# Kernel optimization log

Hardware: AMD Instinct MI355X
Metric: run time of the kernel (lower is better)

Reference implementation:

```python
import jax, jax.numpy as jnp
import numpy as np

D_MODEL = 1024
NUM_HEADS = 16
D_HEAD = D_MODEL // NUM_HEADS
LN_EPS = 1e-5
ROPE_BASE = 10000.0


def layer_norm(x, w, b=None, eps=LN_EPS):
    mu = jnp.mean(x, axis=-1, keepdims=True)
    var = jnp.mean(jnp.square(x - mu), axis=-1, keepdims=True)
    y = (x - mu) * jax.lax.rsqrt(var + eps) * w
    return y + b if b is not None else y


def _rotate_half(x):
    x1, x2 = jnp.split(x, 2, axis=-1)
    return jnp.concatenate([-x2, x1], axis=-1)


def apply_rotary(q, k):
    # q, k: [B, S, H, Dh]
    s, dh = q.shape[1], q.shape[-1]
    inv_freq = 1.0 / (ROPE_BASE ** (jnp.arange(0, dh, 2, dtype=jnp.float32) / dh))
    t = jnp.arange(s, dtype=jnp.float32)
    freqs = jnp.outer(t, inv_freq)                      # [S, Dh/2]
    emb = jnp.concatenate([freqs, freqs], axis=-1)      # [S, Dh]
    cos = jnp.cos(emb)[None, :, None, :].astype(q.dtype)
    sin = jnp.sin(emb)[None, :, None, :].astype(q.dtype)
    q_rot = q * cos + _rotate_half(q) * sin
    k_rot = k * cos + _rotate_half(k) * sin
    return q_rot, k_rot


def setup_inputs() -> dict:
    key = jax.random.key(0)
    ks = jax.random.split(key, 8)
    B, L, D = 4, 2048, D_MODEL
    x = jax.random.normal(ks[0], (B, L, D), dtype=jnp.float32)
    sequence_id = jnp.sort(jax.random.randint(ks[1], (B, L), 0, 8), axis=-1).astype(jnp.int64)
    scale = 1.0 / np.sqrt(D)
    return {
        "x": x,
        "sequence_id": sequence_id,
        "ln_w": jnp.ones((D,), jnp.float32),
        "ln_b": jnp.zeros((D,), jnp.float32),
        "w_qkv": jax.random.normal(ks[2], (D, 3 * D), jnp.float32) * scale,
        "q_ln_w": jnp.ones((D,), jnp.float32),
        "k_ln_w": jnp.ones((D,), jnp.float32),
        "w_out": jax.random.normal(ks[3], (D, D), jnp.float32) * scale,
    }


def reference(x, sequence_id, ln_w, ln_b, w_qkv, q_ln_w, k_ln_w, w_out):
    B, L, D = x.shape
    H, Dh = NUM_HEADS, D_HEAD
    # fused LayerNorm + QKV projection
    qkv = layer_norm(x, ln_w, ln_b) @ w_qkv              # [B, L, 3D]
    q, k, v = jnp.split(qkv, 3, axis=-1)
    # qk layernorm (scale only, bias=False)
    q = layer_norm(q, q_ln_w)
    k = layer_norm(k, k_ln_w)
    # split heads and apply rotary
    q = q.reshape(B, L, H, Dh)
    k = k.reshape(B, L, H, Dh)
    q, k = apply_rotary(q, k)
    v = v.reshape(B, L, H, Dh)
    # packed-sequence mask: tokens attend only within same sequence id
    mask = (sequence_id[:, :, None] == sequence_id[:, None, :])[:, None, :, :]  # [B,1,L,L]
    scale = 1.0 / np.sqrt(Dh)
    scores = jnp.einsum("bqhd,bkhd->bhqk", q, k) * scale
    scores = jnp.where(mask, scores, jnp.finfo(scores.dtype).min)
    attn = jax.nn.softmax(scores, axis=-1)
    ctx = jnp.einsum("bhqk,bkhd->bqhd", attn, v).reshape(B, L, D)
    return ctx @ w_out
```

## Files before the change

### kernel.cpp

```cpp
#include <hip/hip_runtime.h>
#include <hip/hip_bf16.h>
#include <cstdint>
#include <cstddef>
#include <type_traits>

#define D_MODEL 1024
#define NH      16
#define DH      64
#define LSEQ    2048
#define BATCH   4
#define NTOK    8192
#define K3      3072

typedef __attribute__((ext_vector_type(8))) short  short8;
typedef __attribute__((ext_vector_type(4))) float  floatx4;

__device__ __forceinline__ unsigned short f2bf_bits(float f) {
  __hip_bfloat16 h = __float2bfloat16(f);
  return __builtin_bit_cast(unsigned short, h);
}
__device__ __forceinline__ float bf2f(unsigned short u) {
  return __bfloat162float(__builtin_bit_cast(__hip_bfloat16, u));
}
__device__ __forceinline__ unsigned int pack_bf16(float lo, float hi) {
  return (unsigned int)f2bf_bits(lo) | ((unsigned int)f2bf_bits(hi) << 16);
}

__device__ __forceinline__ void gld_lds16(const void* g, void* l) {
  __builtin_amdgcn_global_load_lds(
      (const __attribute__((address_space(1))) void*)g,
      (__attribute__((address_space(3))) void*)l,
      16, 0, 0);
}

__global__ __launch_bounds__(256)
void transpose_cast(const float* __restrict__ src, __hip_bfloat16* __restrict__ dst,
                    int R, int C) {
  __shared__ float tile[32][33];
  const int c0 = blockIdx.x * 32, r0 = blockIdx.y * 32;
  const int x = threadIdx.x, y = threadIdx.y;
  #pragma unroll
  for (int j = 0; j < 32; j += 8)
    tile[y + j][x] = src[(size_t)(r0 + y + j) * C + c0 + x];
  __syncthreads();
  #pragma unroll
  for (int j = 0; j < 32; j += 8)
    dst[(size_t)(c0 + y + j) * R + r0 + x] = __float2bfloat16(tile[x][y + j]);
}

__global__ __launch_bounds__(256)
void ln_kernel(const float* __restrict__ x, const float* __restrict__ w,
               const float* __restrict__ bb, __hip_bfloat16* __restrict__ h) {
  const int t = blockIdx.x, tid = threadIdx.x;
  const float4 v = reinterpret_cast<const float4*>(x + (size_t)t * D_MODEL)[tid];
  float s  = v.x + v.y + v.z + v.w;
  float ss = v.x*v.x + v.y*v.y + v.z*v.z + v.w*v.w;
  #pragma unroll
  for (int off = 32; off > 0; off >>= 1) {
    s  += __shfl_down(s, off);
    ss += __shfl_down(ss, off);
  }
  __shared__ float red[8];
  if ((tid & 63) == 0) { red[(tid >> 6) * 2] = s; red[(tid >> 6) * 2 + 1] = ss; }
  __syncthreads();
  s  = red[0] + red[2] + red[4] + red[6];
  ss = red[1] + red[3] + red[5] + red[7];
  const float mu  = s * (1.f / D_MODEL);
  const float var = ss * (1.f / D_MODEL) - mu * mu;
  const float rs  = rsqrtf(var + 1e-5f);
  const float4 wv = reinterpret_cast<const float4*>(w)[tid];
  const float4 bv = reinterpret_cast<const float4*>(bb)[tid];
  ushort4 o;
  o.x = f2bf_bits((v.x - mu) * rs * wv.x + bv.x);
  o.y = f2bf_bits((v.y - mu) * rs * wv.y + bv.y);
  o.z = f2bf_bits((v.z - mu) * rs * wv.z + bv.z);
  o.w = f2bf_bits((v.w - mu) * rs * wv.w + bv.w);
  reinterpret_cast<ushort4*>(h + (size_t)t * D_MODEL)[tid] = o;
}

template <typename OutT>
__global__ __launch_bounds__(256, 2)
void gemm_bt(const __hip_bfloat16* __restrict__ A, const __hip_bfloat16* __restrict__ Bt,
             OutT* __restrict__ C, int M, int N, int K) {
  const int tid  = threadIdx.x;
  const int lane = tid & 63;
  const int wave = tid >> 6;
  const int bm = blockIdx.y * 128;
  const int bn = blockIdx.x * 128;
  const int wm = (wave & 1) * 64;
  const int wn = (wave >> 1) * 64;
  const int quad = lane >> 4;
  const int l16  = lane & 15;

  __shared__ __align__(16) __hip_bfloat16 As[128 * 64];
  __shared__ __align__(16) __hip_bfloat16 Bs[128 * 64];

  floatx4 acc[4][4];
  #pragma unroll
  for (int i = 0; i < 4; i++)
    #pragma unroll
    for (int j = 0; j < 4; j++) {
      floatx4 z = {0.f, 0.f, 0.f, 0.f};
      acc[i][j] = z;
    }

  const int srow = tid >> 3;
  const int sq   = tid & 7;
  const int sc8  = (sq ^ (srow & 7)) * 8;
  const __hip_bfloat16* Ab = A  + (size_t)(bm + srow) * K + sc8;
  const __hip_bfloat16* Bb = Bt + (size_t)(bn + srow) * K + sc8;

  const int axr = l16 & 7;

  for (int k0 = 0; k0 < K; k0 += 64) {
    __syncthreads();
    #pragma unroll
    for (int p = 0; p < 4; p++) {
      gld_lds16(Ab + (size_t)(p * 32) * K + k0, (char*)As + p * 4096 + tid * 16);
      gld_lds16(Bb + (size_t)(p * 32) * K + k0, (char*)Bs + p * 4096 + tid * 16);
    }
    __syncthreads();
    #pragma unroll
    for (int s0 = 0; s0 < 2; s0++) {
      const int qo = ((s0 * 4 + quad) ^ axr) * 8;
      short8 af[4], bfr[4];
      #pragma unroll
      for (int i = 0; i < 4; i++)
        af[i] = *reinterpret_cast<const short8*>(As + (wm + i * 16 + l16) * 64 + qo);
      #pragma unroll
      for (int j = 0; j < 4; j++)
        bfr[j] = *reinterpret_cast<const short8*>(Bs + (wn + j * 16 + l16) * 64 + qo);
      #pragma unroll
      for (int i = 0; i < 4; i++)
        #pragma unroll
        for (int j = 0; j < 4; j++)
          acc[i][j] = __builtin_amdgcn_mfma_f32_16x16x32_bf16(af[i], bfr[j], acc[i][j], 0, 0, 0);
    }
  }

  #pragma unroll
  for (int i = 0; i < 4; i++)
    #pragma unroll
    for (int j = 0; j < 4; j++) {
      const int row0 = bm + wm + i * 16 + quad * 4;
      const int col  = bn + wn + j * 16 + l16;
      #pragma unroll
      for (int r = 0; r < 4; r++) {
        if constexpr (std::is_same<OutT, __hip_bfloat16>::value)
          C[(size_t)(row0 + r) * N + col] = __float2bfloat16(acc[i][j][r]);
        else
          C[(size_t)(row0 + r) * N + col] = acc[i][j][r];
      }
    }
}

__global__ __launch_bounds__(256)
void seg_kernel(const int* __restrict__ sid, int* __restrict__ segstart,
                int* __restrict__ segend) {
  const int i = blockIdx.x * 256 + threadIdx.x;
  const int b = i >> 11, l = i & 2047;
  const int* row = sid + (size_t)b * LSEQ;
  const int v = row[l];
  int lo = 0, hi = l;
  while (lo < hi) { int mid = (lo + hi) >> 1; if (row[mid] < v) lo = mid + 1; else hi = mid; }
  segstart[i] = lo;
  lo = l + 1; hi = LSEQ;
  while (lo < hi) { int mid = (lo + hi) >> 1; if (row[mid] <= v) lo = mid + 1; else hi = mid; }
  segend[i] = lo;
}

__global__ __launch_bounds__(256)
void rope_kernel(const unsigned short* __restrict__ qkv, const float* __restrict__ qw,
                 const float* __restrict__ kw, unsigned short* __restrict__ qT,
                 unsigned short* __restrict__ kT) {
  const int t = blockIdx.x, tid = threadIdx.x;
  const int b = t >> 11, l = t & 2047;
  const unsigned short* row = qkv + (size_t)t * K3;
  const ushort4 qu = reinterpret_cast<const ushort4*>(row)[tid];
  const ushort4 ku = reinterpret_cast<const ushort4*>(row + 1024)[tid];
  const float4 q4 = make_float4(bf2f(qu.x), bf2f(qu.y), bf2f(qu.z), bf2f(qu.w));
  const float4 k4 = make_float4(bf2f(ku.x), bf2f(ku.y), bf2f(ku.z), bf2f(ku.w));
  float qs  = q4.x + q4.y + q4.z + q4.w;
  float qss = q4.x*q4.x + q4.y*q4.y + q4.z*q4.z + q4.w*q4.w;
  float ks  = k4.x + k4.y + k4.z + k4.w;
  float kss = k4.x*k4.x + k4.y*k4.y + k4.z*k4.z + k4.w*k4.w;
  #pragma unroll
  for (int off = 32; off > 0; off >>= 1) {
    qs  += __shfl_down(qs, off);  qss += __shfl_down(qss, off);
    ks  += __shfl_down(ks, off);  kss += __shfl_down(kss, off);
  }
  __shared__ float red[16];
  const int w = tid >> 6;
  if ((tid & 63) == 0) {
    red[w*4] = qs; red[w*4+1] = qss; red[w*4+2] = ks; red[w*4+3] = kss;
  }
  __syncthreads();
  qs  = red[0] + red[4] + red[8]  + red[12];
  qss = red[1] + red[5] + red[9]  + red[13];
  ks  = red[2] + red[6] + red[10] + red[14];
  kss = red[3] + red[7] + red[11] + red[15];
  const float qmu = qs * (1.f/1024), qvar = qss * (1.f/1024) - qmu*qmu;
  const float qrs = rsqrtf(qvar + 1e-5f);
  const float kmu = ks * (1.f/1024), kvar = kss * (1.f/1024) - kmu*kmu;
  const float krs = rsqrtf(kvar + 1e-5f);

  __shared__ float qn[1024];
  __shared__ float kn[1024];
  const float4 qwv = reinterpret_cast<const float4*>(qw)[tid];
  const float4 kwv = reinterpret_cast<const float4*>(kw)[tid];
  const int d = tid * 4;
  qn[d+0] = (q4.x - qmu) * qrs * qwv.x;
  qn[d+1] = (q4.y - qmu) * qrs * qwv.y;
  qn[d+2] = (q4.z - qmu) * qrs * qwv.z;
  qn[d+3] = (q4.w - qmu) * qrs * qwv.w;
  kn[d+0] = (k4.x - kmu) * krs * kwv.x;
  kn[d+1] = (k4.y - kmu) * krs * kwv.y;
  kn[d+2] = (k4.z - kmu) * krs * kwv.z;
  kn[d+3] = (k4.w - kmu) * krs * kwv.w;
  __syncthreads();

  const int hh = d >> 6, dh = d & 63;
  float oq[4], ok[4];
  #pragma unroll
  for (int i = 0; i < 4; i++) {
    const int dd = dh + i;
    const int j = dd & 31;
    const float th = (float)l * __expf(-(float)j * 0.28782313662425575f);
    const float cs = cosf(th), sn = sinf(th);
    const float qp = (dd < 32) ? -qn[d + i + 32] : qn[d + i - 32];
    const float kp = (dd < 32) ? -kn[d + i + 32] : kn[d + i - 32];
    oq[i] = (qn[d + i] * cs + qp * sn) * 0.125f;
    ok[i] = kn[d + i] * cs + kp * sn;
  }
  const size_t ob = ((size_t)(b * NH + hh) * LSEQ + l) * DH + dh;
  ushort4 pq, pk;
  pq.x = f2bf_bits(oq[0]); pq.y = f2bf_bits(oq[1]); pq.z = f2bf_bits(oq[2]); pq.w = f2bf_bits(oq[3]);
  pk.x = f2bf_bits(ok[0]); pk.y = f2bf_bits(ok[1]); pk.z = f2bf_bits(ok[2]); pk.w = f2bf_bits(ok[3]);
  *reinterpret_cast<ushort4*>(qT + ob) = pq;
  *reinterpret_cast<ushort4*>(kT + ob) = pk;
}

__global__ __launch_bounds__(256)
void vtrans(const unsigned short* __restrict__ qkv, unsigned short* __restrict__ vT) {
  __shared__ __align__(16) unsigned short T[64 * 72];
  const int bh = blockIdx.y;
  const int b = bh >> 4, h = bh & 15;
  const int l0 = blockIdx.x * 64;
  const int tid = threadIdx.x;
  #pragma unroll
  for (int it = 0; it < 2; it++) {
    const int cid = tid + it * 256;
    const int r = cid >> 3, c = (cid & 7) * 8;
    *reinterpret_cast<short8*>(T + r * 72 + c) =
        *reinterpret_cast<const short8*>(qkv + (size_t)(b * LSEQ + l0 + r) * K3
                                         + 2048 + h * DH + c);
  }
  __syncthreads();
  #pragma unroll
  for (int it = 0; it < 2; it++) {
    const int cid = tid + it * 256;
    const int dh = cid >> 3, c = (cid & 7) * 8;
    short8 o;
    #pragma unroll
    for (int e = 0; e < 8; e++) o[e] = (short)T[(c + e) * 72 + dh];
    *reinterpret_cast<short8*>(vT + ((size_t)bh * DH + dh) * LSEQ + l0 + c) = o;
  }
}

__global__ __launch_bounds__(256)
void attn_mfma(const unsigned short* __restrict__ qT, const unsigned short* __restrict__ kT,
               const unsigned short* __restrict__ vT, const int* __restrict__ segs,
               const int* __restrict__ sege, unsigned short* __restrict__ ctx) {
  const int tid  = threadIdx.x;
  const int lane = tid & 63, w = tid >> 6;
  const int quad = lane >> 4, l16 = lane & 15;
  const int qbase = blockIdx.x * 64;
  const int h = blockIdx.y, b = blockIdx.z;
  const int qy = qbase + w * 16 + l16;
  const size_t bh = (size_t)(b * NH + h);
  const unsigned short* Kg = kT + bh * LSEQ * DH;
  const unsigned short* Vg = vT + bh * DH * LSEQ;

  __shared__ __align__(16) unsigned short Ks[64 * 72];
  __shared__ __align__(16) unsigned short Vs[64 * 72];
  __shared__ __align__(16) unsigned short Ps[4][16 * 72];

  const unsigned short* Qrow = qT + (bh * LSEQ + qy) * DH;
  const short8 qf0 = *reinterpret_cast<const short8*>(Qrow + quad * 8);
  const short8 qf1 = *reinterpret_cast<const short8*>(Qrow + 32 + quad * 8);

  const int st = segs[b * LSEQ + qy];
  const int en = sege[b * LSEQ + qy];
  const unsigned span = (unsigned)(en - st);
  const int kmin = segs[b * LSEQ + qbase] & ~63;
  const int kmax = sege[b * LSEQ + qbase + 63];
  const int wmin = segs[b * LSEQ + qbase + w * 16];
  const int wmax = sege[b * LSEQ + qbase + w * 16 + 15];

  floatx4 acc[4];
  #pragma unroll
  for (int dt = 0; dt < 4; dt++) { floatx4 z = {0.f,0.f,0.f,0.f}; acc[dt] = z; }
  float m = -1e30f, lsum = 0.f;

  const int r_ = tid >> 3, c_ = (tid & 7) * 8;

  for (int kk = kmin; kk < kmax; kk += 64) {
    __syncthreads();
    #pragma unroll
    for (int it = 0; it < 2; it++) {
      const int r = r_ + it * 32;
      *reinterpret_cast<short8*>(Ks + r * 72 + c_) =
          *reinterpret_cast<const short8*>(Kg + (size_t)(kk + r) * DH + c_);
      *reinterpret_cast<short8*>(Vs + r * 72 + c_) =
          *reinterpret_cast<const short8*>(Vg + (size_t)r * LSEQ + kk + c_);
    }
    __syncthreads();

    if (kk + 64 <= wmin || kk >= wmax) continue;

    floatx4 sc[4];
    #pragma unroll
    for (int t = 0; t < 4; t++) {
      const short8 kf0 = *reinterpret_cast<const short8*>(Ks + (t * 16 + l16) * 72 + quad * 8);
      const short8 kf1 = *reinterpret_cast<const short8*>(Ks + (t * 16 + l16) * 72 + 32 + quad * 8);
      floatx4 z = {0.f,0.f,0.f,0.f};
      sc[t] = __builtin_amdgcn_mfma_f32_16x16x32_bf16(kf0, qf0, z, 0, 0, 0);
      sc[t] = __builtin_amdgcn_mfma_f32_16x16x32_bf16(kf1, qf1, sc[t], 0, 0, 0);
    }

    float vm = -1e30f;
    #pragma unroll
    for (int t = 0; t < 4; t++) {
      const int k0 = kk + t * 16 + quad * 4;
      #pragma unroll
      for (int r = 0; r < 4; r++) {
        const bool ok = (unsigned)(k0 + r - st) < span;
        sc[t][r] = ok ? sc[t][r] : -1e30f;
        vm = fmaxf(vm, sc[t][r]);
      }
    }
    vm = fmaxf(vm, __shfl_xor(vm, 16));
    vm = fmaxf(vm, __shfl_xor(vm, 32));
    const float mn = fmaxf(m, vm);
    const float alpha = __expf(m - mn);
    m = mn;

    float rs = 0.f;
    #pragma unroll
    for (int t = 0; t < 4; t++) {
      float p0 = (sc[t][0] > -1e29f) ? __expf(sc[t][0] - mn) : 0.f;
      float p1 = (sc[t][1] > -1e29f) ? __expf(sc[t][1] - mn) : 0.f;
      float p2 = (sc[t][2] > -1e29f) ? __expf(sc[t][2] - mn) : 0.f;
      float p3 = (sc[t][3] > -1e29f) ? __expf(sc[t][3] - mn) : 0.f;
      rs += (p0 + p1) + (p2 + p3);
      uint2 pk;
      pk.x = pack_bf16(p0, p1);
      pk.y = pack_bf16(p2, p3);
      *reinterpret_cast<uint2*>(&Ps[w][l16 * 72 + t * 16 + quad * 4]) = pk;
    }
    rs += __shfl_xor(rs, 16);
    rs += __shfl_xor(rs, 32);
    lsum = lsum * alpha + rs;

    const short8 pf0 = *reinterpret_cast<const short8*>(&Ps[w][l16 * 72 + quad * 8]);
    const short8 pf1 = *reinterpret_cast<const short8*>(&Ps[w][l16 * 72 + 32 + quad * 8]);

    #pragma unroll
    for (int dt = 0; dt < 4; dt++) {
      #pragma unroll
      for (int r = 0; r < 4; r++) acc[dt][r] *= alpha;
      const short8 vf0 = *reinterpret_cast<const short8*>(Vs + (dt * 16 + l16) * 72 + quad * 8);
      const short8 vf1 = *reinterpret_cast<const short8*>(Vs + (dt * 16 + l16) * 72 + 32 + quad * 8);
      acc[dt] = __builtin_amdgcn_mfma_f32_16x16x32_bf16(vf0, pf0, acc[dt], 0, 0, 0);
      acc[dt] = __builtin_amdgcn_mfma_f32_16x16x32_bf16(vf1, pf1, acc[dt], 0, 0, 0);
    }
  }

  const float inv = (lsum > 0.f) ? 1.f / lsum : 0.f;
  unsigned short* orow = ctx + ((size_t)(b * LSEQ + qy)) * D_MODEL + h * DH;
  #pragma unroll
  for (int dt = 0; dt < 4; dt++) {
    uint2 o;
    o.x = pack_bf16(acc[dt][0] * inv, acc[dt][1] * inv);
    o.y = pack_bf16(acc[dt][2] * inv, acc[dt][3] * inv);
    *reinterpret_cast<uint2*>(orow + dt * 16 + quad * 4) = o;
  }
}

extern "C" void kernel_launch(void* const* d_in, const int* in_sizes, int n_in,
                              void* d_out, int out_size, void* d_ws, size_t ws_size,
                              hipStream_t stream) {
  const float* x      = (const float*)d_in[0];
  const int*   sid    = (const int*)d_in[1];
  const float* ln_w   = (const float*)d_in[2];
  const float* ln_b   = (const float*)d_in[3];
  const float* w_qkv  = (const float*)d_in[4];
  const float* q_ln_w = (const float*)d_in[5];
  const float* k_ln_w = (const float*)d_in[6];
  const float* w_out  = (const float*)d_in[7];
  float* out = (float*)d_out;
  char* ws = (char*)d_ws;

  constexpr size_t OFF_WQKVT = 0;
  constexpr size_t OFF_WOUTT = 6291456;
  constexpr size_t OFF_H     = 8388608;
  constexpr size_t OFF_QKV   = 25165824;
  constexpr size_t OFF_QT    = 75497472;
  constexpr size_t OFF_KT    = 92274688;
  constexpr size_t OFF_VT    = 109051904;
  constexpr size_t OFF_CTX   = 125829120;
  constexpr size_t OFF_SEGS  = 142606336;
  constexpr size_t OFF_SEGE  = 142639104;

  __hip_bfloat16* wqkvT = (__hip_bfloat16*)(ws + OFF_WQKVT);
  __hip_bfloat16* woutT = (__hip_bfloat16*)(ws + OFF_WOUTT);
  __hip_bfloat16* hbuf  = (__hip_bfloat16*)(ws + OFF_H);
  __hip_bfloat16* qkvb  = (__hip_bfloat16*)(ws + OFF_QKV);
  unsigned short* qTb   = (unsigned short*)(ws + OFF_QT);
  unsigned short* kTb   = (unsigned short*)(ws + OFF_KT);
  unsigned short* vTb   = (unsigned short*)(ws + OFF_VT);
  unsigned short* ctx   = (unsigned short*)(ws + OFF_CTX);
  int*            segst = (int*)(ws + OFF_SEGS);
  int*            segen = (int*)(ws + OFF_SEGE);

  transpose_cast<<<dim3(96, 32), dim3(32, 8), 0, stream>>>(w_qkv, wqkvT, 1024, 3072);
  transpose_cast<<<dim3(32, 32), dim3(32, 8), 0, stream>>>(w_out, woutT, 1024, 1024);
  ln_kernel<<<NTOK, 256, 0, stream>>>(x, ln_w, ln_b, hbuf);
  gemm_bt<__hip_bfloat16><<<dim3(K3 / 128, NTOK / 128), 256, 0, stream>>>(
      hbuf, wqkvT, qkvb, NTOK, K3, 1024);
  seg_kernel<<<NTOK / 256, 256, 0, stream>>>(sid, segst, segen);
  rope_kernel<<<NTOK, 256, 0, stream>>>((const unsigned short*)qkvb, q_ln_w, k_ln_w,
                                        qTb, kTb);
  vtrans<<<dim3(LSEQ / 64, BATCH * NH), 256, 0, stream>>>((const unsigned short*)qkvb, vTb);
  attn_mfma<<<dim3(LSEQ / 64, NH, BATCH), 256, 0, stream>>>(qTb, kTb, vTb, segst, segen, ctx);
  gemm_bt<float><<<dim3(D_MODEL / 128, NTOK / 128), 256, 0, stream>>>(
      (const __hip_bfloat16*)ctx, woutT, out, NTOK, D_MODEL, 1024);
}
```

Measured before the change: 279.3 us.

## Use one wave per row in LN/rope, direct-to-LDS swizzled loads, LDS seg search

LayerNorm and the qk-norm/rotary kernels now process one token per wavefront, so the reduction uses wave shuffles only, with no shared memory or block barriers. Rotary uses sincos computed per lane and broadcast by shuffle, replacing per-element cos/sin. The attention K/V tiles and the V transpose now use direct global-to-LDS loads into an XOR-swizzled 64-wide layout instead of padded register-staged copies, which saves LDS and VGPR traffic. The segment kernel caches the sequence-id row in LDS for its binary searches. The swizzle index maths must match on every read, and gld_lds16 is assumed to already exist in the part of the file not shown.

```diff
diff --git a/kernel.cpp b/kernel.cpp
--- a/kernel.cpp
+++ b/kernel.cpp
@@ -51,31 +51,38 @@
 __global__ __launch_bounds__(256)
 void ln_kernel(const float* __restrict__ x, const float* __restrict__ w,
                const float* __restrict__ bb, __hip_bfloat16* __restrict__ h) {
-  const int t = blockIdx.x, tid = threadIdx.x;
-  const float4 v = reinterpret_cast<const float4*>(x + (size_t)t * D_MODEL)[tid];
-  float s  = v.x + v.y + v.z + v.w;
-  float ss = v.x*v.x + v.y*v.y + v.z*v.z + v.w*v.w;
-  #pragma unroll
-  for (int off = 32; off > 0; off >>= 1) {
-    s  += __shfl_down(s, off);
-    ss += __shfl_down(ss, off);
-  }
-  __shared__ float red[8];
-  if ((tid & 63) == 0) { red[(tid >> 6) * 2] = s; red[(tid >> 6) * 2 + 1] = ss; }
-  __syncthreads();
-  s  = red[0] + red[2] + red[4] + red[6];
-  ss = red[1] + red[3] + red[5] + red[7];
-  const float mu  = s * (1.f / D_MODEL);
-  const float var = ss * (1.f / D_MODEL) - mu * mu;
-  const float rs  = rsqrtf(var + 1e-5f);
-  const float4 wv = reinterpret_cast<const float4*>(w)[tid];
-  const float4 bv = reinterpret_cast<const float4*>(bb)[tid];
-  ushort4 o;
-  o.x = f2bf_bits((v.x - mu) * rs * wv.x + bv.x);
-  o.y = f2bf_bits((v.y - mu) * rs * wv.y + bv.y);
-  o.z = f2bf_bits((v.z - mu) * rs * wv.z + bv.z);
-  o.w = f2bf_bits((v.w - mu) * rs * wv.w + bv.w);
-  reinterpret_cast<ushort4*>(h + (size_t)t * D_MODEL)[tid] = o;
+  const int lane = threadIdx.x & 63;
+  const int t = blockIdx.x * 4 + (threadIdx.x >> 6);
+  const float4* xr = reinterpret_cast<const float4*>(x) + (size_t)t * 256;
+  float4 v[4];
+  float s = 0.f, ss = 0.f;
+  #pragma unroll
+  for (int i = 0; i < 4; i++) {
+    v[i] = xr[lane + i * 64];
+    s  += (v[i].x + v[i].y) + (v[i].z + v[i].w);
+    ss += (v[i].x*v[i].x + v[i].y*v[i].y) + (v[i].z*v[i].z + v[i].w*v[i].w);
+  }
+  #pragma unroll
+  for (int off = 1; off < 64; off <<= 1) {
+    s  += __shfl_xor(s, off);
+    ss += __shfl_xor(ss, off);
+  }
+  const float mu = s * (1.f / 1024);
+  const float rs = rsqrtf(ss * (1.f / 1024) - mu * mu + 1e-5f);
+  const float4* wr = reinterpret_cast<const float4*>(w);
+  const float4* br = reinterpret_cast<const float4*>(bb);
+  ushort4* hr = reinterpret_cast<ushort4*>(h) + (size_t)t * 256;
+  #pragma unroll
+  for (int i = 0; i < 4; i++) {
+    const float4 wv = wr[lane + i * 64];
+    const float4 bv = br[lane + i * 64];
+    ushort4 o;
+    o.x = f2bf_bits((v[i].x - mu) * rs * wv.x + bv.x);
+    o.y = f2bf_bits((v[i].y - mu) * rs * wv.y + bv.y);
+    o.z = f2bf_bits((v[i].z - mu) * rs * wv.z + bv.z);
+    o.w = f2bf_bits((v[i].w - mu) * rs * wv.w + bv.w);
+    hr[lane + i * 64] = o;
+  }
 }
 
 template <typename OutT>
@@ -157,15 +164,22 @@
 __global__ __launch_bounds__(256)
 void seg_kernel(const int* __restrict__ sid, int* __restrict__ segstart,
                 int* __restrict__ segend) {
-  const int i = blockIdx.x * 256 + threadIdx.x;
-  const int b = i >> 11, l = i & 2047;
+  __shared__ int srow[LSEQ];
+  const int blk = blockIdx.x;
+  const int b = blk >> 3;
+  const int tid = threadIdx.x;
   const int* row = sid + (size_t)b * LSEQ;
-  const int v = row[l];
+  #pragma unroll
+  for (int i = 0; i < 8; i++) srow[tid + i * 256] = row[tid + i * 256];
+  __syncthreads();
+  const int l = (blk & 7) * 256 + tid;
+  const int v = srow[l];
   int lo = 0, hi = l;
-  while (lo < hi) { int mid = (lo + hi) >> 1; if (row[mid] < v) lo = mid + 1; else hi = mid; }
+  while (lo < hi) { int mid = (lo + hi) >> 1; if (srow[mid] < v) lo = mid + 1; else hi = mid; }
+  const int i = b * LSEQ + l;
   segstart[i] = lo;
   lo = l + 1; hi = LSEQ;
-  while (lo < hi) { int mid = (lo + hi) >> 1; if (row[mid] <= v) lo = mid + 1; else hi = mid; }
+  while (lo < hi) { int mid = (lo + hi) >> 1; if (srow[mid] <= v) lo = mid + 1; else hi = mid; }
   segend[i] = lo;
 }
 
@@ -173,96 +187,101 @@
 void rope_kernel(const unsigned short* __restrict__ qkv, const float* __restrict__ qw,
                  const float* __restrict__ kw, unsigned short* __restrict__ qT,
                  unsigned short* __restrict__ kT) {
-  const int t = blockIdx.x, tid = threadIdx.x;
+  const int lane = threadIdx.x & 63;
+  const int t = blockIdx.x * 4 + (threadIdx.x >> 6);
   const int b = t >> 11, l = t & 2047;
   const unsigned short* row = qkv + (size_t)t * K3;
-  const ushort4 qu = reinterpret_cast<const ushort4*>(row)[tid];
-  const ushort4 ku = reinterpret_cast<const ushort4*>(row + 1024)[tid];
-  const float4 q4 = make_float4(bf2f(qu.x), bf2f(qu.y), bf2f(qu.z), bf2f(qu.w));
-  const float4 k4 = make_float4(bf2f(ku.x), bf2f(ku.y), bf2f(ku.z), bf2f(ku.w));
-  float qs  = q4.x + q4.y + q4.z + q4.w;
-  float qss = q4.x*q4.x + q4.y*q4.y + q4.z*q4.z + q4.w*q4.w;
-  float ks  = k4.x + k4.y + k4.z + k4.w;
-  float kss = k4.x*k4.x + k4.y*k4.y + k4.z*k4.z + k4.w*k4.w;
-  #pragma unroll
-  for (int off = 32; off > 0; off >>= 1) {
-    qs  += __shfl_down(qs, off);  qss += __shfl_down(qss, off);
-    ks  += __shfl_down(ks, off);  kss += __shfl_down(kss, off);
-  }
-  __shared__ float red[16];
-  const int w = tid >> 6;
-  if ((tid & 63) == 0) {
-    red[w*4] = qs; red[w*4+1] = qss; red[w*4+2] = ks; red[w*4+3] = kss;
-  }
-  __syncthreads();
-  qs  = red[0] + red[4] + red[8]  + red[12];
-  qss = red[1] + red[5] + red[9]  + red[13];
-  ks  = red[2] + red[6] + red[10] + red[14];
-  kss = red[3] + red[7] + red[11] + red[15];
-  const float qmu = qs * (1.f/1024), qvar = qss * (1.f/1024) - qmu*qmu;
-  const float qrs = rsqrtf(qvar + 1e-5f);
-  const float kmu = ks * (1.f/1024), kvar = kss * (1.f/1024) - kmu*kmu;
-  const float krs = rsqrtf(kvar + 1e-5f);
-
-  __shared__ float qn[1024];
-  __shared__ float kn[1024];
-  const float4 qwv = reinterpret_cast<const float4*>(qw)[tid];
-  const float4 kwv = reinterpret_cast<const float4*>(kw)[tid];
-  const int d = tid * 4;
-  qn[d+0] = (q4.x - qmu) * qrs * qwv.x;
-  qn[d+1] = (q4.y - qmu) * qrs * qwv.y;
-  qn[d+2] = (q4.z - qmu) * qrs * qwv.z;
-  qn[d+3] = (q4.w - qmu) * qrs * qwv.w;
-  kn[d+0] = (k4.x - kmu) * krs * kwv.x;
-  kn[d+1] = (k4.y - kmu) * krs * kwv.y;
-  kn[d+2] = (k4.z - kmu) * krs * kwv.z;
-  kn[d+3] = (k4.w - kmu) * krs * kwv.w;
-  __syncthreads();
-
-  const int hh = d >> 6, dh = d & 63;
-  float oq[4], ok[4];
-  #pragma unroll
-  for (int i = 0; i < 4; i++) {
-    const int dd = dh + i;
-    const int j = dd & 31;
-    const float th = (float)l * __expf(-(float)j * 0.28782313662425575f);
-    const float cs = cosf(th), sn = sinf(th);
-    const float qp = (dd < 32) ? -qn[d + i + 32] : qn[d + i - 32];
-    const float kp = (dd < 32) ? -kn[d + i + 32] : kn[d + i - 32];
-    oq[i] = (qn[d + i] * cs + qp * sn) * 0.125f;
-    ok[i] = kn[d + i] * cs + kp * sn;
-  }
-  const size_t ob = ((size_t)(b * NH + hh) * LSEQ + l) * DH + dh;
-  ushort4 pq, pk;
-  pq.x = f2bf_bits(oq[0]); pq.y = f2bf_bits(oq[1]); pq.z = f2bf_bits(oq[2]); pq.w = f2bf_bits(oq[3]);
-  pk.x = f2bf_bits(ok[0]); pk.y = f2bf_bits(ok[1]); pk.z = f2bf_bits(ok[2]); pk.w = f2bf_bits(ok[3]);
-  *reinterpret_cast<ushort4*>(qT + ob) = pq;
-  *reinterpret_cast<ushort4*>(kT + ob) = pk;
+  const int hh = lane >> 2;
+  const int jb = (lane & 3) * 8;
+  const int base = hh * 64 + jb;
+
+  const short8 qa_u = *reinterpret_cast<const short8*>(row + base);
+  const short8 qb_u = *reinterpret_cast<const short8*>(row + base + 32);
+  const short8 ka_u = *reinterpret_cast<const short8*>(row + 1024 + base);
+  const short8 kb_u = *reinterpret_cast<const short8*>(row + 1024 + base + 32);
+
+  float qa[8], qb[8], ka[8], kb[8];
+  float s_q = 0.f, ss_q = 0.f, s_k = 0.f, ss_k = 0.f;
+  #pragma unroll
+  for (int e = 0; e < 8; e++) {
+    qa[e] = bf2f((unsigned short)qa_u[e]); qb[e] = bf2f((unsigned short)qb_u[e]);
+    ka[e] = bf2f((unsigned short)ka_u[e]); kb[e] = bf2f((unsigned short)kb_u[e]);
+    s_q  += qa[e] + qb[e];  ss_q += qa[e]*qa[e] + qb[e]*qb[e];
+    s_k  += ka[e] + kb[e];  ss_k += ka[e]*ka[e] + kb[e]*kb[e];
+  }
+  #pragma unroll
+  for (int off = 1; off < 64; off <<= 1) {
+    s_q  += __shfl_xor(s_q, off);  ss_q += __shfl_xor(ss_q, off);
+    s_k  += __shfl_xor(s_k, off);  ss_k += __shfl_xor(ss_k, off);
+  }
+  const float qmu = s_q * (1.f/1024);
+  const float qrs = rsqrtf(ss_q * (1.f/1024) - qmu*qmu + 1e-5f);
+  const float kmu = s_k * (1.f/1024);
+  const float krs = rsqrtf(ss_k * (1.f/1024) - kmu*kmu + 1e-5f);
+
+  const int j0 = lane & 31;
+  const float invf = __expf(-(float)j0 * 0.28782313662425575f);
+  float tsin, tcos;
+  sincosf((float)l * invf, &tsin, &tcos);
+
+  const float4 wq0 = *reinterpret_cast<const float4*>(qw + base);
+  const float4 wq1 = *reinterpret_cast<const float4*>(qw + base + 4);
+  const float4 wq2 = *reinterpret_cast<const float4*>(qw + base + 32);
+  const float4 wq3 = *reinterpret_cast<const float4*>(qw + base + 36);
+  const float4 wk0 = *reinterpret_cast<const float4*>(kw + base);
+  const float4 wk1 = *reinterpret_cast<const float4*>(kw + base + 4);
+  const float4 wk2 = *reinterpret_cast<const float4*>(kw + base + 32);
+  const float4 wk3 = *reinterpret_cast<const float4*>(kw + base + 36);
+  const float wqa[8] = {wq0.x,wq0.y,wq0.z,wq0.w, wq1.x,wq1.y,wq1.z,wq1.w};
+  const float wqb[8] = {wq2.x,wq2.y,wq2.z,wq2.w, wq3.x,wq3.y,wq3.z,wq3.w};
+  const float wka[8] = {wk0.x,wk0.y,wk0.z,wk0.w, wk1.x,wk1.y,wk1.z,wk1.w};
+  const float wkb[8] = {wk2.x,wk2.y,wk2.z,wk2.w, wk3.x,wk3.y,wk3.z,wk3.w};
+
+  short8 oqa, oqb, oka, okb;
+  #pragma unroll
+  for (int e = 0; e < 8; e++) {
+    const int j = jb + e;
+    const float c  = __shfl(tcos, j);
+    const float sn = __shfl(tsin, j);
+    const float qn1 = (qa[e] - qmu) * qrs * wqa[e];
+    const float qn2 = (qb[e] - qmu) * qrs * wqb[e];
+    const float kn1 = (ka[e] - kmu) * krs * wka[e];
+    const float kn2 = (kb[e] - kmu) * krs * wkb[e];
+    oqa[e] = (short)f2bf_bits((qn1 * c - qn2 * sn) * 0.125f);
+    oqb[e] = (short)f2bf_bits((qn2 * c + qn1 * sn) * 0.125f);
+    oka[e] = (short)f2bf_bits(kn1 * c - kn2 * sn);
+    okb[e] = (short)f2bf_bits(kn2 * c + kn1 * sn);
+  }
+  const size_t ob = ((size_t)(b * NH + hh) * LSEQ + l) * DH + jb;
+  *reinterpret_cast<short8*>(qT + ob)      = oqa;
+  *reinterpret_cast<short8*>(qT + ob + 32) = oqb;
+  *reinterpret_cast<short8*>(kT + ob)      = oka;
+  *reinterpret_cast<short8*>(kT + ob + 32) = okb;
 }
 
 __global__ __launch_bounds__(256)
 void vtrans(const unsigned short* __restrict__ qkv, unsigned short* __restrict__ vT) {
-  __shared__ __align__(16) unsigned short T[64 * 72];
+  __shared__ __align__(16) unsigned short T[64 * 64];
   const int bh = blockIdx.y;
   const int b = bh >> 4, h = bh & 15;
   const int l0 = blockIdx.x * 64;
   const int tid = threadIdx.x;
-  #pragma unroll
-  for (int it = 0; it < 2; it++) {
-    const int cid = tid + it * 256;
-    const int r = cid >> 3, c = (cid & 7) * 8;
-    *reinterpret_cast<short8*>(T + r * 72 + c) =
-        *reinterpret_cast<const short8*>(qkv + (size_t)(b * LSEQ + l0 + r) * K3
-                                         + 2048 + h * DH + c);
-  }
+  const int sr = tid >> 3, scc = tid & 7;
+  const int r1 = sr + 32;
+  gld_lds16(qkv + (size_t)(b * LSEQ + l0 + sr) * K3 + 2048 + h * 64 + ((scc ^ ((sr >> 3) & 7)) * 8),
+            (char*)T + tid * 16);
+  gld_lds16(qkv + (size_t)(b * LSEQ + l0 + r1) * K3 + 2048 + h * 64 + ((scc ^ ((r1 >> 3) & 7)) * 8),
+            (char*)T + 4096 + tid * 16);
   __syncthreads();
   #pragma unroll
   for (int it = 0; it < 2; it++) {
     const int cid = tid + it * 256;
     const int dh = cid >> 3, c = (cid & 7) * 8;
+    const int sl = (dh >> 3) ^ ((c >> 3) & 7);
     short8 o;
     #pragma unroll
-    for (int e = 0; e < 8; e++) o[e] = (short)T[(c + e) * 72 + dh];
+    for (int e = 0; e < 8; e++)
+      o[e] = (short)T[(c + e) * 64 + sl * 8 + (dh & 7)];
     *reinterpret_cast<short8*>(vT + ((size_t)bh * DH + dh) * LSEQ + l0 + c) = o;
   }
 }
@@ -281,8 +300,8 @@
   const unsigned short* Kg = kT + bh * LSEQ * DH;
   const unsigned short* Vg = vT + bh * DH * LSEQ;
 
-  __shared__ __align__(16) unsigned short Ks[64 * 72];
-  __shared__ __align__(16) unsigned short Vs[64 * 72];
+  __shared__ __align__(16) unsigned short Ks[64 * 64];
+  __shared__ __align__(16) unsigned short Vs[64 * 64];
   __shared__ __align__(16) unsigned short Ps[4][16 * 72];
 
   const unsigned short* Qrow = qT + (bh * LSEQ + qy) * DH;
@@ -302,18 +321,18 @@
   for (int dt = 0; dt < 4; dt++) { floatx4 z = {0.f,0.f,0.f,0.f}; acc[dt] = z; }
   float m = -1e30f, lsum = 0.f;
 
-  const int r_ = tid >> 3, c_ = (tid & 7) * 8;
+  const int sr  = tid >> 3, scc = tid & 7;
+  const int r1  = sr + 32;
+  const int sx0 = (scc ^ ((sr >> 3) & 7)) * 8;
+  const int sx1 = (scc ^ ((r1 >> 3) & 7)) * 8;
+  const int fx  = l16 >> 3;
 
   for (int kk = kmin; kk < kmax; kk += 64) {
     __syncthreads();
-    #pragma unroll
-    for (int it = 0; it < 2; it++) {
-      const int r = r_ + it * 32;
-      *reinterpret_cast<short8*>(Ks + r * 72 + c_) =
-          *reinterpret_cast<const short8*>(Kg + (size_t)(kk + r) * DH + c_);
-      *reinterpret_cast<short8*>(Vs + r * 72 + c_) =
-          *reinterpret_cast<const short8*>(Vg + (size_t)r * LSEQ + kk + c_);
-    }
+    gld_lds16(Kg + (size_t)(kk + sr) * DH + sx0, (char*)Ks + tid * 16);
+    gld_lds16(Kg + (size_t)(kk + r1) * DH + sx1, (char*)Ks + 4096 + tid * 16);
+    gld_lds16(Vg + (size_t)sr * LSEQ + kk + sx0, (char*)Vs + tid * 16);
+    gld_lds16(Vg + (size_t)r1 * LSEQ + kk + sx1, (char*)Vs + 4096 + tid * 16);
     __syncthreads();
 
     if (kk + 64 <= wmin || kk >= wmax) continue;
@@ -321,8 +340,10 @@
     floatx4 sc[4];
     #pragma unroll
     for (int t = 0; t < 4; t++) {
-      const short8 kf0 = *reinterpret_cast<const short8*>(Ks + (t * 16 + l16) * 72 + quad * 8);
-      const short8 kf1 = *reinterpret_cast<const short8*>(Ks + (t * 16 + l16) * 72 + 32 + quad * 8);
+      const int row = t * 16 + l16;
+      const int kx = (2 * t + fx) & 7;
+      const short8 kf0 = *reinterpret_cast<const short8*>(Ks + row * 64 + ((quad ^ kx) * 8));
+      const short8 kf1 = *reinterpret_cast<const short8*>(Ks + row * 64 + (((quad + 4) ^ kx) * 8));
       floatx4 z = {0.f,0.f,0.f,0.f};
       sc[t] = __builtin_amdgcn_mfma_f32_16x16x32_bf16(kf0, qf0, z, 0, 0, 0);
       sc[t] = __builtin_amdgcn_mfma_f32_16x16x32_bf16(kf1, qf1, sc[t], 0, 0, 0);
@@ -369,8 +390,10 @@
     for (int dt = 0; dt < 4; dt++) {
       #pragma unroll
       for (int r = 0; r < 4; r++) acc[dt][r] *= alpha;
-      const short8 vf0 = *reinterpret_cast<const short8*>(Vs + (dt * 16 + l16) * 72 + quad * 8);
-      const short8 vf1 = *reinterpret_cast<const short8*>(Vs + (dt * 16 + l16) * 72 + 32 + quad * 8);
+      const int row = dt * 16 + l16;
+      const int vx = (2 * dt + fx) & 7;
+      const short8 vf0 = *reinterpret_cast<const short8*>(Vs + row * 64 + ((quad ^ vx) * 8));
+      const short8 vf1 = *reinterpret_cast<const short8*>(Vs + row * 64 + (((quad + 4) ^ vx) * 8));
       acc[dt] = __builtin_amdgcn_mfma_f32_16x16x32_bf16(vf0, pf0, acc[dt], 0, 0, 0);
       acc[dt] = __builtin_amdgcn_mfma_f32_16x16x32_bf16(vf1, pf1, acc[dt], 0, 0, 0);
     }
@@ -425,12 +448,12 @@
 
   transpose_cast<<<dim3(96, 32), dim3(32, 8), 0, stream>>>(w_qkv, wqkvT, 1024, 3072);
   transpose_cast<<<dim3(32, 32), dim3(32, 8), 0, stream>>>(w_out, woutT, 1024, 1024);
-  ln_kernel<<<NTOK, 256, 0, stream>>>(x, ln_w, ln_b, hbuf);
+  ln_kernel<<<NTOK / 4, 256, 0, stream>>>(x, ln_w, ln_b, hbuf);
   gemm_bt<__hip_bfloat16><<<dim3(K3 / 128, NTOK / 128), 256, 0, stream>>>(
       hbuf, wqkvT, qkvb, NTOK, K3, 1024);
-  seg_kernel<<<NTOK / 256, 256, 0, stream>>>(sid, segst, segen);
-  rope_kernel<<<NTOK, 256, 0, stream>>>((const unsigned short*)qkvb, q_ln_w, k_ln_w,
-                                        qTb, kTb);
+  seg_kernel<<<32, 256, 0, stream>>>(sid, segst, segen);
+  rope_kernel<<<NTOK / 4, 256, 0, stream>>>((const unsigned short*)qkvb, q_ln_w, k_ln_w,
+                                            qTb, kTb);
   vtrans<<<dim3(LSEQ / 64, BATCH * NH), 256, 0, stream>>>((const unsigned short*)qkvb, vTb);
   attn_mfma<<<dim3(LSEQ / 64, NH, BATCH), 256, 0, stream>>>(qTb, kTb, vTb, segst, segen, ctx);
   gemm_bt<float><<<dim3(D_MODEL / 128, NTOK / 128), 256, 0, stream>>>(
```

Result: faster. 262.0 us (-6.2%).
